# Kernel optimization log

Hardware: AMD Instinct MI355X
Metric: run time of the kernel (lower is better)

Reference implementation:

```python
import jax, jax.numpy as jnp
import numpy as np

F, K = 8, 16          # nfieldvars, nkernels
Y, X, P, T = 16, 16, 32, 8  # plats, plons, plevs, ptimes
B = 64                # nbatch


def setup_inputs() -> dict:
    key = jax.random.key(0)
    ks = jax.random.split(key, 9)
    return {
        "patch": jax.random.normal(ks[0], (B, F, Y, X, P, T), dtype=jnp.float32),
        "quadweights": jax.random.uniform(ks[1], (Y, X, P, T), dtype=jnp.float32),
        "mu_lat": 0.1 * jax.random.normal(ks[2], (F, K), dtype=jnp.float32),
        "logsigma_lat": 0.1 * jax.random.normal(ks[3], (F, K), dtype=jnp.float32),
        "mu_lon": 0.1 * jax.random.normal(ks[4], (F, K), dtype=jnp.float32),
        "logsigma_lon": 0.1 * jax.random.normal(ks[5], (F, K), dtype=jnp.float32),
        "mu_lev": 0.1 * jax.random.normal(ks[6], (F, K), dtype=jnp.float32),
        "logsigma_lev": 0.1 * jax.random.normal(ks[7], (F, K), dtype=jnp.float32),
        "logtau_time": 0.1 * jax.random.normal(ks[8], (F, K), dtype=jnp.float32),
    }


def _gaussian1d(length, mu, logsigma, dtype):
    # -> (F, K, length)
    coord = jnp.linspace(-1.0, 1.0, length, dtype=dtype)
    sigma = jnp.exp(logsigma)
    return jnp.exp(-0.5 * ((coord[None, None, :] - mu[..., None]) / sigma[..., None]) ** 2)


def _exponential1d(length, logtau, dtype):
    # -> (F, K, length)
    coord = jnp.arange(length, dtype=dtype)
    tau = jnp.exp(logtau) + 1e-6
    return jnp.exp(-coord[None, None, :] / tau[..., None])


def reference(patch, quadweights, mu_lat, logsigma_lat, mu_lon, logsigma_lon,
              mu_lev, logsigma_lev, logtau_time):
    dt = patch.dtype
    klat = _gaussian1d(Y, mu_lat, logsigma_lat, dt)       # (F,K,Y)
    klon = _gaussian1d(X, mu_lon, logsigma_lon, dt)       # (F,K,X)
    klev = _gaussian1d(P, mu_lev, logsigma_lev, dt)       # (F,K,P)
    ktime = _exponential1d(T, logtau_time, dt)            # (F,K,T)
    # separable outer product -> (F,K,Y,X,P,T)
    kernelparams = (klat[:, :, :, None, None, None]
                    * klon[:, :, None, :, None, None]
                    * klev[:, :, None, None, :, None]
                    * ktime[:, :, None, None, None, :])
    integrated = jnp.einsum('fkyxpt,yxpt->fk', kernelparams, quadweights) + 1e-4
    kernelweights = kernelparams / integrated[:, :, None, None, None, None]
    features = jnp.einsum('bfyxpt,fkyxpt,yxpt->bfk', patch, kernelweights, quadweights)
    return features.reshape(patch.shape[0], F * K)
```

## Files before the change

kernel.cpp:

```cpp
#include <hip/hip_runtime.h>

#define NF 8
#define NK 16
#define NY 16
#define NX 16
#define NP 32
#define NT 8
#define NYX 256
#define NPT 256
#define NB 64

__global__ __launch_bounds__(256) void prep_kernel(
    const float* __restrict__ qw,
    const float* __restrict__ mu_lat, const float* __restrict__ ls_lat,
    const float* __restrict__ mu_lon, const float* __restrict__ ls_lon,
    const float* __restrict__ mu_lev, const float* __restrict__ ls_lev,
    const float* __restrict__ lt_time,
    float* __restrict__ Ag, float* __restrict__ Bg)
{
    const int fk  = blockIdx.x;
    const int tid = threadIdx.x;

    __shared__ float klat[NY];
    __shared__ float klon[NX];
    __shared__ float klev[NP];
    __shared__ float ktim[NT];
    __shared__ float wred[4];
    __shared__ float s_inv;

    if (tid < 16) {
        float c = -1.0f + 2.0f * (float)tid / 15.0f;
        float d = (c - mu_lat[fk]) / expf(ls_lat[fk]);
        klat[tid] = expf(-0.5f * d * d);
    } else if (tid < 32) {
        int i = tid - 16;
        float c = -1.0f + 2.0f * (float)i / 15.0f;
        float d = (c - mu_lon[fk]) / expf(ls_lon[fk]);
        klon[i] = expf(-0.5f * d * d);
    } else if (tid < 64) {
        int i = tid - 32;
        float c = -1.0f + 2.0f * (float)i / 31.0f;
        float d = (c - mu_lev[fk]) / expf(ls_lev[fk]);
        klev[i] = expf(-0.5f * d * d);
    } else if (tid < 72) {
        int i = tid - 64;
        float tau = expf(lt_time[fk]) + 1e-6f;
        ktim[i] = expf(-(float)i / tau);
    }
    __syncthreads();

    const int pt = tid;
    const float bm = klev[pt >> 3] * ktim[pt & 7];

    float acc = 0.0f;
    for (int e = 0; e < NYX; ++e) {
        float a = klat[e >> 4] * klon[e & 15];
        acc = fmaf(qw[e * NPT + pt] * bm, a, acc);
    }
    #pragma unroll
    for (int s = 32; s > 0; s >>= 1) acc += __shfl_xor(acc, s, 64);
    if ((tid & 63) == 0) wred[tid >> 6] = acc;
    __syncthreads();
    if (tid == 0) {
        float integ = wred[0] + wred[1] + wred[2] + wred[3] + 1e-4f;
        s_inv = 1.0f / integ;
    }
    __syncthreads();

    Bg[fk * NPT + pt] = bm;
    Ag[fk * NYX + tid] = klat[tid >> 4] * klon[tid & 15] * s_inv;
}

__global__ __launch_bounds__(256) void main_kernel(
    const float* __restrict__ patch,
    const float* __restrict__ qw,
    const float* __restrict__ Ag,
    const float* __restrict__ Bg,
    float* __restrict__ out)
{
    const int chunk = blockIdx.x;
    const int f     = blockIdx.y;
    const int b     = blockIdx.z;
    const int tid   = threadIdx.x;
    const int lane  = tid & 63;
    const int wid   = tid >> 6;

    float4 bm4[NK];
    #pragma unroll
    for (int k = 0; k < NK; ++k)
        bm4[k] = *reinterpret_cast<const float4*>(Bg + ((f * NK + k) << 8) + (lane << 2));

    float acc[NK];
    #pragma unroll
    for (int k = 0; k < NK; ++k) acc[k] = 0.0f;

    const size_t pb  = ((size_t)(b * NF + f)) << 16;
    const int   yx0  = chunk * 64 + wid * 16;

    for (int g = 0; g < 4; ++g) {
        const int yx = yx0 + g * 4;
        float4 wp[4];
        #pragma unroll
        for (int j = 0; j < 4; ++j) {
            const int off = ((yx + j) << 8) + (lane << 2);
            float4 p = *reinterpret_cast<const float4*>(patch + pb + off);
            float4 q = *reinterpret_cast<const float4*>(qw + off);
            wp[j].x = p.x * q.x;
            wp[j].y = p.y * q.y;
            wp[j].z = p.z * q.z;
            wp[j].w = p.w * q.w;
        }
        #pragma unroll
        for (int k = 0; k < NK; ++k) {
            const float4 a4 = *reinterpret_cast<const float4*>(Ag + ((f * NK + k) << 8) + yx);
            float i0 = fmaf(wp[0].x, bm4[k].x, fmaf(wp[0].y, bm4[k].y, fmaf(wp[0].z, bm4[k].z, wp[0].w * bm4[k].w)));
            float i1 = fmaf(wp[1].x, bm4[k].x, fmaf(wp[1].y, bm4[k].y, fmaf(wp[1].z, bm4[k].z, wp[1].w * bm4[k].w)));
            float i2 = fmaf(wp[2].x, bm4[k].x, fmaf(wp[2].y, bm4[k].y, fmaf(wp[2].z, bm4[k].z, wp[2].w * bm4[k].w)));
            float i3 = fmaf(wp[3].x, bm4[k].x, fmaf(wp[3].y, bm4[k].y, fmaf(wp[3].z, bm4[k].z, wp[3].w * bm4[k].w)));
            float s = fmaf(a4.x, i0, fmaf(a4.y, i1, fmaf(a4.z, i2, a4.w * i3)));
            acc[k] += s;
        }
    }

    #pragma unroll
    for (int k = 0; k < NK; ++k) {
        float v = acc[k];
        #pragma unroll
        for (int s = 32; s > 0; s >>= 1) v += __shfl_xor(v, s, 64);
        acc[k] = v;
    }

    if (lane == 0) {
        #pragma unroll
        for (int k = 0; k < NK; ++k)
            atomicAdd(out + (b * NF + f) * NK + k, acc[k]);
    }
}

extern "C" void kernel_launch(void* const* d_in, const int* in_sizes, int n_in,
                              void* d_out, int out_size, void* d_ws, size_t ws_size,
                              hipStream_t stream)
{
    const float* patch   = (const float*)d_in[0];
    const float* qw      = (const float*)d_in[1];
    const float* mu_lat  = (const float*)d_in[2];
    const float* ls_lat  = (const float*)d_in[3];
    const float* mu_lon  = (const float*)d_in[4];
    const float* ls_lon  = (const float*)d_in[5];
    const float* mu_lev  = (const float*)d_in[6];
    const float* ls_lev  = (const float*)d_in[7];
    const float* lt_time = (const float*)d_in[8];
    float* out = (float*)d_out;

    float* Ag = (float*)d_ws;
    float* Bg = Ag + NF * NK * NYX;

    hipMemsetAsync(d_out, 0, (size_t)out_size * sizeof(float), stream);

    prep_kernel<<<dim3(NF * NK), dim3(256), 0, stream>>>(
        qw, mu_lat, ls_lat, mu_lon, ls_lon, mu_lev, ls_lev, lt_time, Ag, Bg);

    main_kernel<<<dim3(4, NF, NB), dim3(256), 0, stream>>>(patch, qw, Ag, Bg, out);
}
```

Baseline: 256.0 us.

## Reorder contraction to apply PT factor after YX reduction, drop atomics

The main kernel now accumulates patch*qw weighted by the yx kernel factor into per-lane float4 accumulators for all 16 kernels. It applies the pt factor only once at the end, which removes the per-iteration dot products against Bg. The yx weights are transposed in the prep kernel and staged in shared memory. Each block now handles a whole (b,f) slice and writes its output directly, so the memset and the atomics go away. The prep kernel's loop is also vectorized. The cost is 4x fewer blocks (512) and more accumulator registers, which could reduce latency hiding.

```diff
diff --git a/kernel.cpp b/kernel.cpp
--- a/kernel.cpp
+++ b/kernel.cpp
@@ -16,15 +16,17 @@
     const float* __restrict__ mu_lon, const float* __restrict__ ls_lon,
     const float* __restrict__ mu_lev, const float* __restrict__ ls_lev,
     const float* __restrict__ lt_time,
-    float* __restrict__ Ag, float* __restrict__ Bg)
+    float* __restrict__ At,
+    float* __restrict__ Bg)
 {
-    const int fk  = blockIdx.x;
-    const int tid = threadIdx.x;
+    const int fk   = blockIdx.x;
+    const int f    = fk >> 4;
+    const int k    = fk & 15;
+    const int tid  = threadIdx.x;
+    const int lane = tid & 63;
+    const int wid  = tid >> 6;
 
-    __shared__ float klat[NY];
-    __shared__ float klon[NX];
-    __shared__ float klev[NP];
-    __shared__ float ktim[NT];
+    __shared__ float klat[NY], klon[NX], klev[NP], ktim[NT];
     __shared__ float wred[4];
     __shared__ float s_inv;
 
@@ -49,92 +51,110 @@
     }
     __syncthreads();
 
-    const int pt = tid;
-    const float bm = klev[pt >> 3] * ktim[pt & 7];
+    const float kl = klev[lane >> 1];
+    float4 bm4;
+    bm4.x = kl * ktim[(lane & 1) * 4 + 0];
+    bm4.y = kl * ktim[(lane & 1) * 4 + 1];
+    bm4.z = kl * ktim[(lane & 1) * 4 + 2];
+    bm4.w = kl * ktim[(lane & 1) * 4 + 3];
 
     float acc = 0.0f;
-    for (int e = 0; e < NYX; ++e) {
-        float a = klat[e >> 4] * klon[e & 15];
-        acc = fmaf(qw[e * NPT + pt] * bm, a, acc);
+    #pragma unroll 4
+    for (int i = 0; i < 64; ++i) {
+        const int yx = wid * 64 + i;
+        float4 q4 = *reinterpret_cast<const float4*>(qw + yx * NPT + (lane << 2));
+        float s = fmaf(q4.x, bm4.x, fmaf(q4.y, bm4.y, fmaf(q4.z, bm4.z, q4.w * bm4.w)));
+        float a = klat[yx >> 4] * klon[yx & 15];
+        acc = fmaf(a, s, acc);
     }
     #pragma unroll
-    for (int s = 32; s > 0; s >>= 1) acc += __shfl_xor(acc, s, 64);
-    if ((tid & 63) == 0) wred[tid >> 6] = acc;
+    for (int s = 32; s; s >>= 1) acc += __shfl_xor(acc, s, 64);
+    if (lane == 0) wred[wid] = acc;
     __syncthreads();
-    if (tid == 0) {
-        float integ = wred[0] + wred[1] + wred[2] + wred[3] + 1e-4f;
-        s_inv = 1.0f / integ;
-    }
+    if (tid == 0) s_inv = 1.0f / (wred[0] + wred[1] + wred[2] + wred[3] + 1e-4f);
     __syncthreads();
 
-    Bg[fk * NPT + pt] = bm;
-    Ag[fk * NYX + tid] = klat[tid >> 4] * klon[tid & 15] * s_inv;
+    Bg[fk * NPT + tid] = klev[tid >> 3] * ktim[tid & 7];
+    At[(f * NYX + tid) * NK + k] = klat[tid >> 4] * klon[tid & 15] * s_inv;
 }
 
 __global__ __launch_bounds__(256) void main_kernel(
     const float* __restrict__ patch,
     const float* __restrict__ qw,
-    const float* __restrict__ Ag,
+    const float* __restrict__ At,
     const float* __restrict__ Bg,
     float* __restrict__ out)
 {
-    const int chunk = blockIdx.x;
-    const int f     = blockIdx.y;
-    const int b     = blockIdx.z;
-    const int tid   = threadIdx.x;
-    const int lane  = tid & 63;
-    const int wid   = tid >> 6;
+    const int bf   = blockIdx.x;
+    const int f    = bf & 7;
+    const int tid  = threadIdx.x;
+    const int lane = tid & 63;
+    const int wid  = tid >> 6;
 
-    float4 bm4[NK];
+    __shared__ float sA[NYX * NK];
+    {
+        const float4* src = reinterpret_cast<const float4*>(At + f * NYX * NK);
+        float4* dst = reinterpret_cast<float4*>(sA);
+        #pragma unroll
+        for (int j = 0; j < 4; ++j)
+            dst[tid + 256 * j] = src[tid + 256 * j];
+    }
+    __syncthreads();
+
+    float4 acc[NK];
     #pragma unroll
-    for (int k = 0; k < NK; ++k)
-        bm4[k] = *reinterpret_cast<const float4*>(Bg + ((f * NK + k) << 8) + (lane << 2));
+    for (int k = 0; k < NK; ++k) acc[k] = make_float4(0.f, 0.f, 0.f, 0.f);
 
-    float acc[NK];
-    #pragma unroll
-    for (int k = 0; k < NK; ++k) acc[k] = 0.0f;
+    const float* pbase = patch + ((size_t)bf << 16);
+    const int row0 = wid * 64;
 
-    const size_t pb  = ((size_t)(b * NF + f)) << 16;
-    const int   yx0  = chunk * 64 + wid * 16;
-
-    for (int g = 0; g < 4; ++g) {
-        const int yx = yx0 + g * 4;
-        float4 wp[4];
+    #pragma unroll 8
+    for (int i = 0; i < 64; ++i) {
+        const int yx  = row0 + i;
+        const int off = (yx << 8) + (lane << 2);
+        float4 p4 = *reinterpret_cast<const float4*>(pbase + off);
+        float4 q4 = *reinterpret_cast<const float4*>(qw + off);
+        float4 wp;
+        wp.x = p4.x * q4.x; wp.y = p4.y * q4.y;
+        wp.z = p4.z * q4.z; wp.w = p4.w * q4.w;
+        const float4* arow = reinterpret_cast<const float4*>(sA + (yx << 4));
         #pragma unroll
-        for (int j = 0; j < 4; ++j) {
-            const int off = ((yx + j) << 8) + (lane << 2);
-            float4 p = *reinterpret_cast<const float4*>(patch + pb + off);
-            float4 q = *reinterpret_cast<const float4*>(qw + off);
-            wp[j].x = p.x * q.x;
-            wp[j].y = p.y * q.y;
-            wp[j].z = p.z * q.z;
-            wp[j].w = p.w * q.w;
-        }
-        #pragma unroll
-        for (int k = 0; k < NK; ++k) {
-            const float4 a4 = *reinterpret_cast<const float4*>(Ag + ((f * NK + k) << 8) + yx);
-            float i0 = fmaf(wp[0].x, bm4[k].x, fmaf(wp[0].y, bm4[k].y, fmaf(wp[0].z, bm4[k].z, wp[0].w * bm4[k].w)));
-            float i1 = fmaf(wp[1].x, bm4[k].x, fmaf(wp[1].y, bm4[k].y, fmaf(wp[1].z, bm4[k].z, wp[1].w * bm4[k].w)));
-            float i2 = fmaf(wp[2].x, bm4[k].x, fmaf(wp[2].y, bm4[k].y, fmaf(wp[2].z, bm4[k].z, wp[2].w * bm4[k].w)));
-            float i3 = fmaf(wp[3].x, bm4[k].x, fmaf(wp[3].y, bm4[k].y, fmaf(wp[3].z, bm4[k].z, wp[3].w * bm4[k].w)));
-            float s = fmaf(a4.x, i0, fmaf(a4.y, i1, fmaf(a4.z, i2, a4.w * i3)));
-            acc[k] += s;
+        for (int kq = 0; kq < 4; ++kq) {
+            const float4 a4 = arow[kq];
+            float4& c0 = acc[kq * 4 + 0];
+            float4& c1 = acc[kq * 4 + 1];
+            float4& c2 = acc[kq * 4 + 2];
+            float4& c3 = acc[kq * 4 + 3];
+            c0.x = fmaf(a4.x, wp.x, c0.x); c0.y = fmaf(a4.x, wp.y, c0.y);
+            c0.z = fmaf(a4.x, wp.z, c0.z); c0.w = fmaf(a4.x, wp.w, c0.w);
+            c1.x = fmaf(a4.y, wp.x, c1.x); c1.y = fmaf(a4.y, wp.y, c1.y);
+            c1.z = fmaf(a4.y, wp.z, c1.z); c1.w = fmaf(a4.y, wp.w, c1.w);
+            c2.x = fmaf(a4.z, wp.x, c2.x); c2.y = fmaf(a4.z, wp.y, c2.y);
+            c2.z = fmaf(a4.z, wp.z, c2.z); c2.w = fmaf(a4.z, wp.w, c2.w);
+            c3.x = fmaf(a4.w, wp.x, c3.x); c3.y = fmaf(a4.w, wp.y, c3.y);
+            c3.z = fmaf(a4.w, wp.z, c3.z); c3.w = fmaf(a4.w, wp.w, c3.w);
         }
     }
 
+    __shared__ float red[4][NK];
+    float v[NK];
     #pragma unroll
     for (int k = 0; k < NK; ++k) {
-        float v = acc[k];
+        const float4 bm4 = *reinterpret_cast<const float4*>(
+            Bg + ((f * NK + k) << 8) + (lane << 2));
+        float s = fmaf(acc[k].x, bm4.x, fmaf(acc[k].y, bm4.y,
+                  fmaf(acc[k].z, bm4.z, acc[k].w * bm4.w)));
         #pragma unroll
-        for (int s = 32; s > 0; s >>= 1) v += __shfl_xor(v, s, 64);
-        acc[k] = v;
+        for (int t = 32; t; t >>= 1) s += __shfl_xor(s, t, 64);
+        v[k] = s;
     }
-
     if (lane == 0) {
         #pragma unroll
-        for (int k = 0; k < NK; ++k)
-            atomicAdd(out + (b * NF + f) * NK + k, acc[k]);
+        for (int k = 0; k < NK; ++k) red[wid][k] = v[k];
     }
+    __syncthreads();
+    if (tid < NK)
+        out[bf * NK + tid] = red[0][tid] + red[1][tid] + red[2][tid] + red[3][tid];
 }
 
 extern "C" void kernel_launch(void* const* d_in, const int* in_sizes, int n_in,
@@ -152,13 +172,11 @@
     const float* lt_time = (const float*)d_in[8];
     float* out = (float*)d_out;
 
-    float* Ag = (float*)d_ws;
-    float* Bg = Ag + NF * NK * NYX;
-
-    hipMemsetAsync(d_out, 0, (size_t)out_size * sizeof(float), stream);
+    float* At = (float*)d_ws;
+    float* Bg = At + NF * NYX * NK;
 
     prep_kernel<<<dim3(NF * NK), dim3(256), 0, stream>>>(
-        qw, mu_lat, ls_lat, mu_lon, ls_lon, mu_lev, ls_lev, lt_time, Ag, Bg);
+        qw, mu_lat, ls_lat, mu_lon, ls_lon, mu_lev, ls_lev, lt_time, At, Bg);
 
-    main_kernel<<<dim3(4, NF, NB), dim3(256), 0, stream>>>(patch, qw, Ag, Bg, out);
+    main_kernel<<<dim3(NB * NF), dim3(256), 0, stream>>>(patch, qw, At, Bg, out);
 }
```

New measurement: 230.3 us. 10.0% less time.
